# Kernel optimization log

Hardware: AMD Instinct MI355X
Metric: run time of the kernel (lower is better)

The kernel has to match this reference:

```python
import jax, jax.numpy as jnp
import numpy as np

TEMPERATURE = 0.07
BASE_TEMPERATURE = 0.07


def _pairwise_euclid(x):
    # torch.cdist(x, x, p=2), with safe sqrt (zero grad at zero distance)
    sq = jnp.sum(x * x, axis=1)
    d2 = sq[:, None] + sq[None, :] - 2.0 * (x @ x.T)
    d2 = jnp.maximum(d2, 0.0)
    safe = jnp.where(d2 > 0.0, d2, 1.0)
    return jnp.where(d2 > 0.0, jnp.sqrt(safe), 0.0)


def setup_inputs() -> dict:
    key = jax.random.key(0)
    k1, k2 = jax.random.split(key)
    features = jax.random.normal(k1, (1024, 2, 512), dtype=jnp.float32)
    labels = jax.random.uniform(k2, (1024,), dtype=jnp.float32)
    return {"features": features, "labels": labels}


def reference(features, labels):
    B, V, D = features.shape
    N = B * V
    # torch.cat(torch.unbind(features, dim=1), dim=0): views stacked -> [N, D]
    cf = features.transpose(1, 0, 2).reshape(N, D)
    lab = jnp.tile(labels, V)  # label of row i is labels[i % B]

    dist = _pairwise_euclid(cf)              # [N, N]
    logits = -dist / TEMPERATURE
    eye = jnp.eye(N, dtype=logits.dtype)
    w = jnp.exp(logits) * (1.0 - eye)        # exp(logits) with l == i excluded

    dis = jnp.abs(lab[:, None] - lab[None, :])  # |y_i - y_j|, symmetric

    # negative[i, j] = sum_{l != i, |y_l - y_i| >= |y_i - y_j|} exp(logits[i, l])
    # computed per-row via sort + suffix cumsum + searchsorted (O(N^2 log N))
    order = jnp.argsort(dis, axis=1)
    sorted_d = jnp.take_along_axis(dis, order, axis=1)
    sorted_w = jnp.take_along_axis(w, order, axis=1)
    suffix = jnp.flip(jnp.cumsum(jnp.flip(sorted_w, axis=1), axis=1), axis=1)
    suffix = jnp.concatenate([suffix, jnp.zeros((N, 1), suffix.dtype)], axis=1)  # [N, N+1]
    # side='left': counts entries strictly < d, so suffix[idx] sums all >= d (ties incl.)
    idx = jax.vmap(lambda sd, d: jnp.searchsorted(sd, d, side='left'))(sorted_d, dis)
    negative = jnp.take_along_axis(suffix, idx, axis=1)
    negative = negative * (1.0 - eye) + eye  # diag set to 1 (log -> 0)

    logits_z = logits * (1.0 - eye)          # logits[i, i] = 0
    log_prob = logits_z - jnp.log(negative)
    mean_log_prob_pos = jnp.sum(log_prob, axis=1) / (N - 1)
    loss = -(TEMPERATURE / BASE_TEMPERATURE) * jnp.mean(mean_log_prob_pos)
    return loss
```

## Files before the change

kernel.cpp:

```cpp
#include <hip/hip_runtime.h>
#include <math.h>


#define NN 2048
#define BB 1024
#define DD 512
#define NT 256
#define NEGINF (-INFINITY)

typedef short s16x8 __attribute__((ext_vector_type(8)));
typedef float f32x4 __attribute__((ext_vector_type(4)));

__device__ __forceinline__ const float* cf_row(const float* F, int i) {
    return F + ((size_t)(i & (BB - 1)) * 2 + (size_t)(i >> 10)) * DD;
}

__device__ __forceinline__ unsigned bf_rne(float x) {
    const unsigned u = __float_as_uint(x);
    return (u + 0x7FFFu + ((u >> 16) & 1u)) >> 16;
}
__device__ __forceinline__ float bf_val(unsigned h) {
    return __uint_as_float(h << 16);
}

__device__ __forceinline__ float dlogf(double s) {
    const unsigned long long b = __double_as_longlong(s);
    const int e2 = (int)(b >> 52) - 1023;
    const double md = __longlong_as_double((b & 0xFFFFFFFFFFFFFULL) | 0x3FF0000000000000ULL);
    return (float)e2 * 0.6931471805599453f + __logf((float)md);
}

__global__ __launch_bounds__(512) void sort_labels_kernel(const float* __restrict__ labels,
                                                          float* __restrict__ slab,
                                                          int* __restrict__ sj,
                                                          int* __restrict__ inv) {
    __shared__ float kk[BB];
    __shared__ int   id[BB];
    const int t = threadIdx.x;
    #pragma unroll
    for (int e = 0; e < 2; ++e) { const int p = t + e * 512; kk[p] = labels[p]; id[p] = p; }
    for (int k = 2; k <= BB; k <<= 1) {
        for (int j = k >> 1; j > 0; j >>= 1) {
            __syncthreads();
            #pragma unroll
            for (int e = 0; e < 2; ++e) {
                const int idx = t + e * 512;
                const int ixj = idx ^ j;
                if (ixj > idx) {
                    const float k1 = kk[idx], k2 = kk[ixj];
                    const bool up = ((idx & k) == 0);
                    if (up ? (k1 > k2) : (k1 < k2)) {
                        kk[idx] = k2; kk[ixj] = k1;
                        const int i1 = id[idx]; id[idx] = id[ixj]; id[ixj] = i1;
                    }
                }
            }
        }
    }
    __syncthreads();
    #pragma unroll
    for (int e = 0; e < 2; ++e) {
        const int p = t + e * 512;
        const float lv = kk[p];
        const int b = id[p];
        slab[2 * p] = lv; slab[2 * p + 1] = lv;
        sj[2 * p] = b;    sj[2 * p + 1] = b + BB;
        inv[b] = 2 * p;   inv[b + BB] = 2 * p + 1;
    }
}

__global__ __launch_bounds__(256) void prep_split_kernel(const float* __restrict__ F,
                                                         ushort* __restrict__ Ahi,
                                                         ushort* __restrict__ Alo,
                                                         float* __restrict__ sq) {
    const int t = threadIdx.x;
    const int lane = t & 63;
    const int w = t >> 6;
    const int i = blockIdx.x * 4 + w;
    const float* src = cf_row(F, i);
    const float4 v0 = reinterpret_cast<const float4*>(src)[lane];
    const float4 v1 = reinterpret_cast<const float4*>(src)[lane + 64];
    float ss = v0.x * v0.x + v0.y * v0.y + v0.z * v0.z + v0.w * v0.w
             + v1.x * v1.x + v1.y * v1.y + v1.z * v1.z + v1.w * v1.w;
    #pragma unroll
    for (int st = 32; st > 0; st >>= 1) ss += __shfl_down(ss, st);
    if (lane == 0) sq[i] = ss;

    const float a[8] = {v0.x, v0.y, v0.z, v0.w, v1.x, v1.y, v1.z, v1.w};
    ushort h[8], l[8];
    #pragma unroll
    for (int e = 0; e < 8; ++e) {
        const unsigned hb = bf_rne(a[e]);
        h[e] = (ushort)hb;
        l[e] = (ushort)bf_rne(a[e] - bf_val(hb));
    }
    const size_t base = (size_t)i * DD;
    *reinterpret_cast<ushort4*>(&Ahi[base + lane * 4])       = make_ushort4(h[0], h[1], h[2], h[3]);
    *reinterpret_cast<ushort4*>(&Ahi[base + 256 + lane * 4]) = make_ushort4(h[4], h[5], h[6], h[7]);
    *reinterpret_cast<ushort4*>(&Alo[base + lane * 4])       = make_ushort4(l[0], l[1], l[2], l[3]);
    *reinterpret_cast<ushort4*>(&Alo[base + 256 + lane * 4]) = make_ushort4(l[4], l[5], l[6], l[7]);
}

#define TM 128
#define TN 64
#define TK 32
__global__ __launch_bounds__(256) void gemm_dist_kernel(const ushort* __restrict__ Ahi,
                                                        const ushort* __restrict__ Alo,
                                                        const float* __restrict__ sq,
                                                        const int* __restrict__ sj,
                                                        float* __restrict__ distp) {
    __shared__ ushort Ah[4][TM][8];
    __shared__ ushort Al[4][TM][8];
    __shared__ ushort Bh[4][TN][8];
    __shared__ ushort Bl[4][TN][8];
    __shared__ int   sjc[TN];
    __shared__ float sqA[TM];
    __shared__ float sqB[TN];

    const int t = threadIdx.x;
    const int lane = t & 63;
    const int w = t >> 6;
    const int row0 = blockIdx.y * TM;
    const int col0 = blockIdx.x * TN;

    if (t < TN) {
        const int s = sj[col0 + t];
        sjc[t] = s;
        sqB[t] = sq[s];
    } else if (t < TN + TM) {
        sqA[t - TN] = sq[row0 + (t - TN)];
    }

    f32x4 acc[2][4] = {};
    const int m = lane & 15;
    const int q = lane >> 4;

    for (int kt = 0; kt < DD / TK; ++kt) {
        __syncthreads();
        for (int c = t; c < TM * 4; c += NT) {
            const int row = c >> 2, cq = c & 3;
            const size_t g = (size_t)(row0 + row) * DD + kt * TK + cq * 8;
            *reinterpret_cast<int4*>(&Ah[cq][row][0]) = *reinterpret_cast<const int4*>(&Ahi[g]);
            *reinterpret_cast<int4*>(&Al[cq][row][0]) = *reinterpret_cast<const int4*>(&Alo[g]);
        }
        for (int c = t; c < TN * 4; c += NT) {
            const int row = c >> 2, cq = c & 3;
            const size_t g = (size_t)sjc[row] * DD + kt * TK + cq * 8;
            *reinterpret_cast<int4*>(&Bh[cq][row][0]) = *reinterpret_cast<const int4*>(&Ahi[g]);
            *reinterpret_cast<int4*>(&Bl[cq][row][0]) = *reinterpret_cast<const int4*>(&Alo[g]);
        }
        __syncthreads();

        s16x8 fah[2], fal[2], fbh[4], fbl[4];
        #pragma unroll
        for (int mt = 0; mt < 2; ++mt) {
            fah[mt] = *reinterpret_cast<const s16x8*>(&Ah[q][w * 32 + mt * 16 + m][0]);
            fal[mt] = *reinterpret_cast<const s16x8*>(&Al[q][w * 32 + mt * 16 + m][0]);
        }
        #pragma unroll
        for (int nt = 0; nt < 4; ++nt) {
            fbh[nt] = *reinterpret_cast<const s16x8*>(&Bh[q][nt * 16 + m][0]);
            fbl[nt] = *reinterpret_cast<const s16x8*>(&Bl[q][nt * 16 + m][0]);
        }
        #pragma unroll
        for (int mt = 0; mt < 2; ++mt)
            #pragma unroll
            for (int nt = 0; nt < 4; ++nt) {
                acc[mt][nt] = __builtin_amdgcn_mfma_f32_16x16x32_bf16(fah[mt], fbh[nt], acc[mt][nt], 0, 0, 0);
                acc[mt][nt] = __builtin_amdgcn_mfma_f32_16x16x32_bf16(fah[mt], fbl[nt], acc[mt][nt], 0, 0, 0);
                acc[mt][nt] = __builtin_amdgcn_mfma_f32_16x16x32_bf16(fal[mt], fbh[nt], acc[mt][nt], 0, 0, 0);
            }
    }

    #pragma unroll
    for (int mt = 0; mt < 2; ++mt) {
        #pragma unroll
        for (int nt = 0; nt < 4; ++nt) {
            #pragma unroll
            for (int r = 0; r < 4; ++r) {
                const int lr = w * 32 + mt * 16 + q * 4 + r;
                const int lc = nt * 16 + m;
                const float d2 = sqA[lr] + sqB[lc] - 2.0f * acc[mt][nt][r];
                distp[(size_t)(row0 + lr) * NN + col0 + lc] = (d2 > 0.f) ? sqrtf(d2) : 0.f;
            }
        }
    }
}

__device__ __forceinline__ int bs_right(const float* key, float d, int lo, int hi) {
    while (lo < hi) {
        const int mid = (lo + hi) >> 1;
        if (key[mid] >= d) hi = mid; else lo = mid + 1;
    }
    return lo;
}
__device__ __forceinline__ int bs_left(const float* key, float d, int lo, int hi) {
    while (lo < hi) {
        const int mid = (lo + hi) >> 1;
        if (key[mid] < d) hi = mid; else lo = mid + 1;
    }
    return lo;
}

__global__ __launch_bounds__(256) void row_kernel(const float* __restrict__ distp,
                                                  const float* __restrict__ labels,
                                                  const float* __restrict__ slab,
                                                  const int* __restrict__ inv,
                                                  double* __restrict__ rowval) {
    __shared__ float  key[NN];
    __shared__ double Pd[NN];
    __shared__ double Sd[NN + 1];
    __shared__ float  wmx[4];
    __shared__ double wps[4], wss[4], wD[4], wL[4];

    const int i = blockIdx.x;
    const int t = threadIdx.x;
    const int lane = t & 63;
    const int w = t >> 6;
    const int pos_i = inv[i];
    const float x = labels[i & (BB - 1)];
    const float negInvT = -1.0f / 0.07f;
    const float* drow = &distp[(size_t)i * NN];

    #pragma unroll
    for (int e = 0; e < 2; ++e) {
        const int p4 = t + e * NT;
        const float4 l4 = reinterpret_cast<const float4*>(slab)[p4];
        key[p4 * 4 + 0] = fabsf(l4.x - x);
        key[p4 * 4 + 1] = fabsf(l4.y - x);
        key[p4 * 4 + 2] = fabsf(l4.z - x);
        key[p4 * 4 + 3] = fabsf(l4.w - x);
    }
    const int cb = t * 8;
    float v[8];
    double dsum = 0.0;
    float mx = NEGINF;
    #pragma unroll
    for (int e = 0; e < 2; ++e) {
        const float4 d4 = reinterpret_cast<const float4*>(drow)[2 * t + e];
        const float dv[4] = {d4.x, d4.y, d4.z, d4.w};
        #pragma unroll
        for (int c = 0; c < 4; ++c) {
            const int pc = cb + e * 4 + c;
            if (pc == pos_i) {
                v[e * 4 + c] = NEGINF;
            } else {
                const float vv = dv[c] * negInvT;
                v[e * 4 + c] = vv;
                mx = fmaxf(mx, vv);
                dsum += (double)dv[c];
            }
        }
    }
    #pragma unroll
    for (int st = 32; st > 0; st >>= 1) mx = fmaxf(mx, __shfl_down(mx, st));
    if (lane == 0) wmx[w] = mx;
    __syncthreads();
    const float M = fmaxf(fmaxf(wmx[0], wmx[1]), fmaxf(wmx[2], wmx[3]));

    double e8[8];
    #pragma unroll
    for (int jj = 0; jj < 8; ++jj) {
        const float tt = __expf((v[jj] - M) * 0.5f);
        e8[jj] = (double)tt * (double)tt;
    }

    {
        double run = 0.0, ex[8];
        #pragma unroll
        for (int jj = 0; jj < 8; ++jj) { ex[jj] = run; run += e8[jj]; }
        double inc = run;
        #pragma unroll
        for (int st = 1; st < 64; st <<= 1) {
            const double nm = __shfl_up(inc, st);
            if (lane >= st) inc += nm;
        }
        double xofs = __shfl_up(inc, 1);
        if (lane == 0) xofs = 0.0;
        if (lane == 63) wps[w] = inc;
        __syncthreads();
        #pragma unroll
        for (int ww = 0; ww < 3; ++ww)
            if (ww < w) xofs += wps[ww];
        #pragma unroll
        for (int jj = 0; jj < 8; ++jj) Pd[cb + jj] = ex[jj] + xofs;
    }

    {
        double run = 0.0, sx[8];
        #pragma unroll
        for (int jj = 7; jj >= 0; --jj) { run += e8[jj]; sx[jj] = run; }
        double inc = run;
        #pragma unroll
        for (int st = 1; st < 64; st <<= 1) {
            const double nm = __shfl_down(inc, st);
            if (lane + st < 64) inc += nm;
        }
        double xofs = __shfl_down(inc, 1);
        if (lane == 63) xofs = 0.0;
        if (lane == 0) wss[w] = inc;
        __syncthreads();
        #pragma unroll
        for (int ww = 1; ww < 4; ++ww)
            if (ww > w) xofs += wss[ww];
        #pragma unroll
        for (int jj = 0; jj < 8; ++jj) Sd[cb + jj] = sx[jj] + xofs;
        if (t == 0) Sd[NN] = 0.0;
    }
    __syncthreads();

    double lnsum = 0.0;
    const int a = cb, b = cb + 7;
    {
        const int le = (pos_i - 1 < b) ? pos_i - 1 : b;
        if (a <= le) {
            const float da = key[a];
            const int Ra = bs_right(key, da, pos_i, NN);
            int Rl = Ra;
            if (le > a) Rl = bs_right(key, key[le], pos_i, Ra);
            for (int p = a; p <= le; ++p) {
                const float d = key[p];
                int R;
                if (p == a) R = Ra;
                else if (p == le) R = Rl;
                else R = bs_right(key, d, Rl, Ra);
                int L = p + 1;
                while (L < pos_i && key[L] == d) ++L;
                lnsum += (double)(M + dlogf(Pd[L] + Sd[R]));
            }
        }
    }
    {
        const int rs = (pos_i + 1 > a) ? pos_i + 1 : a;
        if (rs <= b) {
            const float dr = key[rs];
            const int Lr = bs_left(key, dr, 0, pos_i);
            int Lb = Lr;
            if (b > rs) Lb = bs_left(key, key[b], 0, Lr);
            for (int p = rs; p <= b; ++p) {
                const float d = key[p];
                int L;
                if (p == rs) L = Lr;
                else if (p == b) L = Lb;
                else L = bs_left(key, d, Lb, Lr);
                int R = p;
                while (R > pos_i && key[R - 1] == d) --R;
                lnsum += (double)(M + dlogf(Pd[L] + Sd[R]));
            }
        }
    }

    #pragma unroll
    for (int st = 32; st > 0; st >>= 1) {
        dsum  += __shfl_down(dsum, st);
        lnsum += __shfl_down(lnsum, st);
    }
    if (lane == 0) { wD[w] = dsum; wL[w] = lnsum; }
    __syncthreads();
    if (t == 0) {
        const double td = wD[0] + wD[1] + wD[2] + wD[3];
        const double tl = wL[0] + wL[1] + wL[2] + wL[3];
        rowval[i] = (-td / 0.07) - tl;
    }
}

__global__ __launch_bounds__(256) void finalize_kernel(const double* __restrict__ rowval,
                                                       float* __restrict__ out) {
    __shared__ double red[NT];
    const int t = threadIdx.x;
    double s = 0.0;
    for (int j = t; j < NN; j += NT) s += rowval[j];
    red[t] = s;
    __syncthreads();
    for (int ofs = NT / 2; ofs > 0; ofs >>= 1) {
        if (t < ofs) red[t] += red[t + ofs];
        __syncthreads();
    }
    if (t == 0) {
        out[0] = (float)(-red[0] / ((double)NN * (double)(NN - 1)));
    }
}

extern "C" void kernel_launch(void* const* d_in, const int* in_sizes, int n_in,
                              void* d_out, int out_size, void* d_ws, size_t ws_size,
                              hipStream_t stream) {
    const float* features = (const float*)d_in[0];
    const float* labels   = (const float*)d_in[1];
    float* out = (float*)d_out;

    char* ws = (char*)d_ws;
    size_t off = 0;
    float*  sq     = (float*) (ws + off); off += NN * sizeof(float);
    float*  slab   = (float*) (ws + off); off += NN * sizeof(float);
    int*    sj     = (int*)   (ws + off); off += NN * sizeof(int);
    int*    inv    = (int*)   (ws + off); off += NN * sizeof(int);
    double* rowval = (double*)(ws + off); off += NN * sizeof(double);
    ushort* Ahi    = (ushort*)(ws + off); off += (size_t)NN * DD * sizeof(ushort);
    ushort* Alo    = (ushort*)(ws + off); off += (size_t)NN * DD * sizeof(ushort);
    float*  distp  = (float*) (ws + off); off += (size_t)NN * NN * sizeof(float);

    sort_labels_kernel<<<1, 512, 0, stream>>>(labels, slab, sj, inv);
    prep_split_kernel<<<NN / 4, NT, 0, stream>>>(features, Ahi, Alo, sq);
    dim3 ggrid(NN / TN, NN / TM);
    gemm_dist_kernel<<<ggrid, NT, 0, stream>>>(Ahi, Alo, sq, sj, distp);
    row_kernel<<<NN, NT, 0, stream>>>(distp, labels, slab, inv, rowval);
    finalize_kernel<<<1, NT, 0, stream>>>(rowval, out);
}
```

Measured before the change: 161.3 us.

## Permute GEMM rows to sorted-label order and switch row prefix sums to fp32

The GEMM now gathers both A and B rows through the sorted-label permutation, so the distance matrix comes out fully in sorted order. The row kernel can then drop the inverse permutation and use the block index as the diagonal position. Prefix and suffix sums of exp weights move from double to float, with a constant shift of 64 to avoid underflow, and the custom double log is replaced by a plain __logf. Inner bitonic-sort stages with small strides use wave barriers instead of block barriers. This lowers fp64 work and shared-memory footprint, at the risk of fp32 accumulation error and overflow or underflow in the weight sums.

```diff
diff --git a/kernel.cpp b/kernel.cpp
--- a/kernel.cpp
+++ b/kernel.cpp
@@ -7,6 +7,7 @@
 #define DD 512
 #define NT 256
 #define NEGINF (-INFINITY)
+#define CS 64.0f
 
 typedef short s16x8 __attribute__((ext_vector_type(8)));
 typedef float f32x4 __attribute__((ext_vector_type(4)));
@@ -23,17 +24,9 @@
     return __uint_as_float(h << 16);
 }
 
-__device__ __forceinline__ float dlogf(double s) {
-    const unsigned long long b = __double_as_longlong(s);
-    const int e2 = (int)(b >> 52) - 1023;
-    const double md = __longlong_as_double((b & 0xFFFFFFFFFFFFFULL) | 0x3FF0000000000000ULL);
-    return (float)e2 * 0.6931471805599453f + __logf((float)md);
-}
-
 __global__ __launch_bounds__(512) void sort_labels_kernel(const float* __restrict__ labels,
                                                           float* __restrict__ slab,
-                                                          int* __restrict__ sj,
-                                                          int* __restrict__ inv) {
+                                                          int* __restrict__ sj) {
     __shared__ float kk[BB];
     __shared__ int   id[BB];
     const int t = threadIdx.x;
@@ -41,7 +34,8 @@
     for (int e = 0; e < 2; ++e) { const int p = t + e * 512; kk[p] = labels[p]; id[p] = p; }
     for (int k = 2; k <= BB; k <<= 1) {
         for (int j = k >> 1; j > 0; j >>= 1) {
-            __syncthreads();
+            if (j >= 32) __syncthreads();
+            else __builtin_amdgcn_wave_barrier();
             #pragma unroll
             for (int e = 0; e < 2; ++e) {
                 const int idx = t + e * 512;
@@ -65,7 +59,6 @@
         const int b = id[p];
         slab[2 * p] = lv; slab[2 * p + 1] = lv;
         sj[2 * p] = b;    sj[2 * p + 1] = b + BB;
-        inv[b] = 2 * p;   inv[b + BB] = 2 * p + 1;
     }
 }
 
@@ -113,7 +106,8 @@
     __shared__ ushort Al[4][TM][8];
     __shared__ ushort Bh[4][TN][8];
     __shared__ ushort Bl[4][TN][8];
-    __shared__ int   sjc[TN];
+    __shared__ int   sjcA[TM];
+    __shared__ int   sjcB[TN];
     __shared__ float sqA[TM];
     __shared__ float sqB[TN];
 
@@ -123,13 +117,20 @@
     const int row0 = blockIdx.y * TM;
     const int col0 = blockIdx.x * TN;
 
-    if (t < TN) {
-        const int s = sj[col0 + t];
-        sjc[t] = s;
-        sqB[t] = sq[s];
-    } else if (t < TN + TM) {
-        sqA[t - TN] = sq[row0 + (t - TN)];
-    }
+    if (t < TM) {
+        const int s = sj[row0 + t];
+        sjcA[t] = s; sqA[t] = sq[s];
+    } else if (t < TM + TN) {
+        const int u = t - TM;
+        const int s = sj[col0 + u];
+        sjcB[u] = s; sqB[u] = sq[s];
+    }
+    __syncthreads();
+    const int rr = t >> 2;
+    const int cq = t & 3;
+    const size_t gA0 = (size_t)sjcA[rr] * DD + cq * 8;
+    const size_t gA1 = (size_t)sjcA[64 + rr] * DD + cq * 8;
+    const size_t gB0 = (size_t)sjcB[rr] * DD + cq * 8;
 
     f32x4 acc[2][4] = {};
     const int m = lane & 15;
@@ -137,18 +138,13 @@
 
     for (int kt = 0; kt < DD / TK; ++kt) {
         __syncthreads();
-        for (int c = t; c < TM * 4; c += NT) {
-            const int row = c >> 2, cq = c & 3;
-            const size_t g = (size_t)(row0 + row) * DD + kt * TK + cq * 8;
-            *reinterpret_cast<int4*>(&Ah[cq][row][0]) = *reinterpret_cast<const int4*>(&Ahi[g]);
-            *reinterpret_cast<int4*>(&Al[cq][row][0]) = *reinterpret_cast<const int4*>(&Alo[g]);
-        }
-        for (int c = t; c < TN * 4; c += NT) {
-            const int row = c >> 2, cq = c & 3;
-            const size_t g = (size_t)sjc[row] * DD + kt * TK + cq * 8;
-            *reinterpret_cast<int4*>(&Bh[cq][row][0]) = *reinterpret_cast<const int4*>(&Ahi[g]);
-            *reinterpret_cast<int4*>(&Bl[cq][row][0]) = *reinterpret_cast<const int4*>(&Alo[g]);
-        }
+        const size_t ko = (size_t)kt * TK;
+        *reinterpret_cast<int4*>(&Ah[cq][rr][0])      = *reinterpret_cast<const int4*>(&Ahi[gA0 + ko]);
+        *reinterpret_cast<int4*>(&Al[cq][rr][0])      = *reinterpret_cast<const int4*>(&Alo[gA0 + ko]);
+        *reinterpret_cast<int4*>(&Ah[cq][64 + rr][0]) = *reinterpret_cast<const int4*>(&Ahi[gA1 + ko]);
+        *reinterpret_cast<int4*>(&Al[cq][64 + rr][0]) = *reinterpret_cast<const int4*>(&Alo[gA1 + ko]);
+        *reinterpret_cast<int4*>(&Bh[cq][rr][0])      = *reinterpret_cast<const int4*>(&Ahi[gB0 + ko]);
+        *reinterpret_cast<int4*>(&Bl[cq][rr][0])      = *reinterpret_cast<const int4*>(&Alo[gB0 + ko]);
         __syncthreads();
 
         s16x8 fah[2], fal[2], fbh[4], fbl[4];
@@ -203,24 +199,21 @@
 }
 
 __global__ __launch_bounds__(256) void row_kernel(const float* __restrict__ distp,
-                                                  const float* __restrict__ labels,
                                                   const float* __restrict__ slab,
-                                                  const int* __restrict__ inv,
                                                   double* __restrict__ rowval) {
-    __shared__ float  key[NN];
-    __shared__ double Pd[NN];
-    __shared__ double Sd[NN + 1];
-    __shared__ float  wmx[4];
-    __shared__ double wps[4], wss[4], wD[4], wL[4];
-
-    const int i = blockIdx.x;
+    __shared__ float key[NN];
+    __shared__ float Pf[NN];
+    __shared__ float Sf[NN + 1];
+    __shared__ float wmx[4], wps[4], wss[4];
+    __shared__ double wD[4], wL[4];
+
+    const int r = blockIdx.x;
     const int t = threadIdx.x;
     const int lane = t & 63;
     const int w = t >> 6;
-    const int pos_i = inv[i];
-    const float x = labels[i & (BB - 1)];
+    const float x = slab[r];
     const float negInvT = -1.0f / 0.07f;
-    const float* drow = &distp[(size_t)i * NN];
+    const float* drow = &distp[(size_t)r * NN];
 
     #pragma unroll
     for (int e = 0; e < 2; ++e) {
@@ -242,7 +235,7 @@
         #pragma unroll
         for (int c = 0; c < 4; ++c) {
             const int pc = cb + e * 4 + c;
-            if (pc == pos_i) {
+            if (pc == r) {
                 v[e * 4 + c] = NEGINF;
             } else {
                 const float vv = dv[c] * negInvT;
@@ -258,66 +251,64 @@
     __syncthreads();
     const float M = fmaxf(fmaxf(wmx[0], wmx[1]), fmaxf(wmx[2], wmx[3]));
 
-    double e8[8];
-    #pragma unroll
-    for (int jj = 0; jj < 8; ++jj) {
-        const float tt = __expf((v[jj] - M) * 0.5f);
-        e8[jj] = (double)tt * (double)tt;
-    }
+    float e8[8];
+    #pragma unroll
+    for (int jj = 0; jj < 8; ++jj) e8[jj] = __expf(v[jj] - M + CS);
 
     {
-        double run = 0.0, ex[8];
+        float run = 0.f, ex[8];
         #pragma unroll
         for (int jj = 0; jj < 8; ++jj) { ex[jj] = run; run += e8[jj]; }
-        double inc = run;
+        float inc = run;
         #pragma unroll
         for (int st = 1; st < 64; st <<= 1) {
-            const double nm = __shfl_up(inc, st);
+            const float nm = __shfl_up(inc, st);
             if (lane >= st) inc += nm;
         }
-        double xofs = __shfl_up(inc, 1);
-        if (lane == 0) xofs = 0.0;
+        float xofs = __shfl_up(inc, 1);
+        if (lane == 0) xofs = 0.f;
         if (lane == 63) wps[w] = inc;
         __syncthreads();
         #pragma unroll
         for (int ww = 0; ww < 3; ++ww)
             if (ww < w) xofs += wps[ww];
         #pragma unroll
-        for (int jj = 0; jj < 8; ++jj) Pd[cb + jj] = ex[jj] + xofs;
+        for (int jj = 0; jj < 8; ++jj) Pf[cb + jj] = ex[jj] + xofs;
     }
 
     {
-        double run = 0.0, sx[8];
+        float run = 0.f, sx[8];
         #pragma unroll
         for (int jj = 7; jj >= 0; --jj) { run += e8[jj]; sx[jj] = run; }
-        double inc = run;
+        float inc = run;
         #pragma unroll
         for (int st = 1; st < 64; st <<= 1) {
-            const double nm = __shfl_down(inc, st);
+            const float nm = __shfl_down(inc, st);
             if (lane + st < 64) inc += nm;
         }
-        double xofs = __shfl_down(inc, 1);
-        if (lane == 63) xofs = 0.0;
+        float xofs = __shfl_down(inc, 1);
+        if (lane == 63) xofs = 0.f;
         if (lane == 0) wss[w] = inc;
         __syncthreads();
         #pragma unroll
         for (int ww = 1; ww < 4; ++ww)
             if (ww > w) xofs += wss[ww];
         #pragma unroll
-        for (int jj = 0; jj < 8; ++jj) Sd[cb + jj] = sx[jj] + xofs;
-        if (t == 0) Sd[NN] = 0.0;
+        for (int jj = 0; jj < 8; ++jj) Sf[cb + jj] = sx[jj] + xofs;
+        if (t == 0) Sf[NN] = 0.f;
     }
     __syncthreads();
 
     double lnsum = 0.0;
     const int a = cb, b = cb + 7;
+    const float MB = M - CS;
     {
-        const int le = (pos_i - 1 < b) ? pos_i - 1 : b;
+        const int le = (r - 1 < b) ? r - 1 : b;
         if (a <= le) {
             const float da = key[a];
-            const int Ra = bs_right(key, da, pos_i, NN);
+            const int Ra = bs_right(key, da, r, NN);
             int Rl = Ra;
-            if (le > a) Rl = bs_right(key, key[le], pos_i, Ra);
+            if (le > a) Rl = bs_right(key, key[le], r, Ra);
             for (int p = a; p <= le; ++p) {
                 const float d = key[p];
                 int R;
@@ -325,16 +316,17 @@
                 else if (p == le) R = Rl;
                 else R = bs_right(key, d, Rl, Ra);
                 int L = p + 1;
-                while (L < pos_i && key[L] == d) ++L;
-                lnsum += (double)(M + dlogf(Pd[L] + Sd[R]));
+                while (L < r && key[L] == d) ++L;
+                const float s = fmaxf(Pf[L] + Sf[R], 1e-38f);
+                lnsum += (double)(MB + __logf(s));
             }
         }
     }
     {
-        const int rs = (pos_i + 1 > a) ? pos_i + 1 : a;
+        const int rs = (r + 1 > a) ? r + 1 : a;
         if (rs <= b) {
             const float dr = key[rs];
-            const int Lr = bs_left(key, dr, 0, pos_i);
+            const int Lr = bs_left(key, dr, 0, r);
             int Lb = Lr;
             if (b > rs) Lb = bs_left(key, key[b], 0, Lr);
             for (int p = rs; p <= b; ++p) {
@@ -344,8 +336,9 @@
                 else if (p == b) L = Lb;
                 else L = bs_left(key, d, Lb, Lr);
                 int R = p;
-                while (R > pos_i && key[R - 1] == d) --R;
-                lnsum += (double)(M + dlogf(Pd[L] + Sd[R]));
+                while (R > r && key[R - 1] == d) --R;
+                const float s = fmaxf(Pf[L] + Sf[R], 1e-38f);
+                lnsum += (double)(MB + __logf(s));
             }
         }
     }
@@ -360,7 +353,7 @@
     if (t == 0) {
         const double td = wD[0] + wD[1] + wD[2] + wD[3];
         const double tl = wL[0] + wL[1] + wL[2] + wL[3];
-        rowval[i] = (-td / 0.07) - tl;
+        rowval[r] = (-td / 0.07) - tl;
     }
 }
 
@@ -393,16 +386,15 @@
     float*  sq     = (float*) (ws + off); off += NN * sizeof(float);
     float*  slab   = (float*) (ws + off); off += NN * sizeof(float);
     int*    sj     = (int*)   (ws + off); off += NN * sizeof(int);
-    int*    inv    = (int*)   (ws + off); off += NN * sizeof(int);
     double* rowval = (double*)(ws + off); off += NN * sizeof(double);
     ushort* Ahi    = (ushort*)(ws + off); off += (size_t)NN * DD * sizeof(ushort);
     ushort* Alo    = (ushort*)(ws + off); off += (size_t)NN * DD * sizeof(ushort);
     float*  distp  = (float*) (ws + off); off += (size_t)NN * NN * sizeof(float);
 
-    sort_labels_kernel<<<1, 512, 0, stream>>>(labels, slab, sj, inv);
+    sort_labels_kernel<<<1, 512, 0, stream>>>(labels, slab, sj);
     prep_split_kernel<<<NN / 4, NT, 0, stream>>>(features, Ahi, Alo, sq);
     dim3 ggrid(NN / TN, NN / TM);
     gemm_dist_kernel<<<ggrid, NT, 0, stream>>>(Ahi, Alo, sq, sj, distp);
-    row_kernel<<<NN, NT, 0, stream>>>(distp, labels, slab, inv, rowval);
+    row_kernel<<<NN, NT, 0, stream>>>(distp, slab, rowval);
     finalize_kernel<<<1, NT, 0, stream>>>(rowval, out);
 }
```

New measurement: 142.6 us. 1.13x faster.
